# Kernel tuning notes

Measured on AMD Instinct MI355X. Metric: run time of the kernel, lower is better.

## Reference

```python
import jax, jax.numpy as jnp
import numpy as np

N_NODES = 100000
N_EDGES = 1600000
N_FEAT = 512
N_HID = 256
N_CLASS = 40


def setup_inputs() -> dict:
    key = jax.random.key(0)
    ks = jax.random.split(key, 6)
    features = jax.random.normal(ks[0], (N_NODES, N_FEAT), dtype=jnp.float32)
    edge_index = jax.random.randint(ks[1], (2, N_EDGES), 0, N_NODES, dtype=jnp.int32)
    edge_weight = jax.random.uniform(ks[2], (N_EDGES,), dtype=jnp.float32)
    # xavier_uniform with gain=1.414 (as in reset_parameters)
    g = 1.414
    lim1 = g * np.sqrt(6.0 / (N_FEAT + N_HID))
    lim2 = g * np.sqrt(6.0 / (N_HID + N_CLASS))
    W1 = jax.random.uniform(ks[3], (N_FEAT, N_HID), minval=-lim1, maxval=lim1, dtype=jnp.float32)
    W2 = jax.random.uniform(ks[4], (N_HID, N_CLASS), minval=-lim2, maxval=lim2, dtype=jnp.float32)
    b1 = jnp.zeros((N_HID,), dtype=jnp.float32)
    b2 = jnp.zeros((N_CLASS,), dtype=jnp.float32)
    return {"features": features, "edge_index": edge_index, "edge_weight": edge_weight,
            "W1": W1, "b1": b1, "W2": W2, "b2": b2}


def _spmm(edge_index, edge_weight, x, n):
    # out[r] = sum over edges e with row[e]==r of w[e] * x[col[e]]
    row, col = edge_index[0], edge_index[1]
    msgs = edge_weight[:, None] * x[col]  # [E, D]
    return jax.ops.segment_sum(msgs, row, num_segments=n)


def reference(features, edge_index, edge_weight, W1, b1, W2, b2):
    n = features.shape[0]
    # Layer 1: linear -> spmm -> relu (dropout is identity in eval mode)
    h = features @ W1 + b1
    h = jax.nn.relu(_spmm(edge_index, edge_weight, h, n))
    # Layer 2: linear -> spmm -> log_softmax
    h = h @ W2 + b2
    h = _spmm(edge_index, edge_weight, h, n)
    return jax.nn.log_softmax(h, axis=1)
```

## Files before the change

### kernel.cpp

```cpp
#include <hip/hip_runtime.h>
#include <stdint.h>

#define N_NODES 100000
#define N_EDGES 1600000
#define N_FEAT 512
#define N_HID 256
#define N_CLASS 40

typedef float f32x4 __attribute__((ext_vector_type(4)));
typedef __bf16 bf16x8 __attribute__((ext_vector_type(8)));
typedef unsigned short u16x4 __attribute__((ext_vector_type(4)));
typedef unsigned short u16x8 __attribute__((ext_vector_type(8)));

__device__ __forceinline__ unsigned short f2bf(float f) {
  unsigned int u = __float_as_uint(f);
  unsigned int r = (u + 0x7FFFu + ((u >> 16) & 1u)) >> 16;
  return (unsigned short)r;
}
__device__ __forceinline__ float bf2f(unsigned short s) {
  return __uint_as_float(((unsigned int)s) << 16);
}

__global__ void k_w1t(const float* __restrict__ W1, unsigned short* __restrict__ W1t) {
  int gid = blockIdx.x * 256 + threadIdx.x;
  if (gid >= N_HID * N_FEAT) return;
  int n = gid / N_FEAT, k = gid % N_FEAT;
  W1t[gid] = f2bf(W1[(long)k * N_HID + n]);
}

__global__ void k_w2t(const float* __restrict__ W2, unsigned short* __restrict__ W2t) {
  int gid = blockIdx.x * 256 + threadIdx.x;
  if (gid >= 48 * N_HID) return;
  int n = gid / N_HID, k = gid % N_HID;
  W2t[gid] = (n < N_CLASS) ? f2bf(W2[(long)k * N_CLASS + n]) : (unsigned short)0;
}

__global__ void k_hist(const int* __restrict__ ei, int* __restrict__ cnt) {
  int e = blockIdx.x * 256 + threadIdx.x;
  if (e < N_EDGES) atomicAdd(&cnt[ei[e]], 1);
}

__global__ __launch_bounds__(1024) void k_scan_a(const int* __restrict__ cnt,
                                                 int* __restrict__ rp,
                                                 int* __restrict__ bsum) {
  __shared__ int sm[1024];
  const int tid = threadIdx.x;
  const int i = blockIdx.x * 1024 + tid;
  int v = (i < N_NODES) ? cnt[i] : 0;
  sm[tid] = v;
  __syncthreads();
  #pragma unroll
  for (int d = 1; d < 1024; d <<= 1) {
    int t = (tid >= d) ? sm[tid - d] : 0;
    __syncthreads();
    sm[tid] += t;
    __syncthreads();
  }
  if (i < N_NODES) rp[i] = sm[tid] - v;
  if (tid == 1023) bsum[blockIdx.x] = sm[1023];
}

__global__ __launch_bounds__(128) void k_scan_b(const int* __restrict__ bsum,
                                                int* __restrict__ boffs,
                                                int* __restrict__ rp) {
  __shared__ int sm[128];
  const int tid = threadIdx.x;
  const int nb = (N_NODES + 1023) >> 10;
  int v = (tid < nb) ? bsum[tid] : 0;
  sm[tid] = v;
  __syncthreads();
  #pragma unroll
  for (int d = 1; d < 128; d <<= 1) {
    int t = (tid >= d) ? sm[tid - d] : 0;
    __syncthreads();
    sm[tid] += t;
    __syncthreads();
  }
  boffs[tid] = sm[tid] - v;
  if (tid == 127) rp[N_NODES] = sm[127];
}

__global__ void k_scan_c(int* __restrict__ rp, int* __restrict__ cur,
                         const int* __restrict__ boffs) {
  int i = blockIdx.x * 256 + threadIdx.x;
  if (i >= N_NODES) return;
  int v = rp[i] + boffs[i >> 10];
  rp[i] = v;
  cur[i] = v;
}

__global__ void k_scatter(const int* __restrict__ ei, const float* __restrict__ ew,
                          int* __restrict__ cursor, int2* __restrict__ cw) {
  int e = blockIdx.x * 256 + threadIdx.x;
  if (e >= N_EDGES) return;
  int r = ei[e];
  int pos = atomicAdd(&cursor[r], 1);
  cw[pos] = make_int2(ei[N_EDGES + e], __float_as_int(ew[e]));
}

__global__ __launch_bounds__(512) void k_gemm1(const float* __restrict__ X,
                                               const unsigned short* __restrict__ W1t,
                                               const float* __restrict__ b1,
                                               unsigned short* __restrict__ H1) {
  __shared__ unsigned short As[128][32];
  __shared__ unsigned short Bs[256][32];
  const int t = threadIdx.x;
  const int lane = t & 63;
  const int wid = t >> 6;
  const int wm = wid >> 2, wn = wid & 3;
  const long m0 = (long)blockIdx.x * 128;

  f32x4 acc[4][4] = {};
  const int ar = t >> 2;
  const int ak = (t & 3) * 8;
  const long arow = m0 + ar;
  const bool avalid = arow < N_NODES;
  const float* xsrc = X + arow * N_FEAT + ak;
  const unsigned short* bsrc0 = W1t + (long)ar * N_FEAT + ak;
  const unsigned short* bsrc1 = W1t + (long)(ar + 128) * N_FEAT + ak;

  for (int k0 = 0; k0 < N_FEAT; k0 += 32) {
    __syncthreads();
    f32x4 x0 = {}, x1 = {};
    if (avalid) {
      x0 = *(const f32x4*)(xsrc + k0);
      x1 = *(const f32x4*)(xsrc + k0 + 4);
    }
    u16x8 ap;
    ap[0] = f2bf(x0[0]); ap[1] = f2bf(x0[1]); ap[2] = f2bf(x0[2]); ap[3] = f2bf(x0[3]);
    ap[4] = f2bf(x1[0]); ap[5] = f2bf(x1[1]); ap[6] = f2bf(x1[2]); ap[7] = f2bf(x1[3]);
    *(u16x8*)&As[ar][ak] = ap;
    *(u16x8*)&Bs[ar][ak]       = *(const u16x8*)(bsrc0 + k0);
    *(u16x8*)&Bs[ar + 128][ak] = *(const u16x8*)(bsrc1 + k0);
    __syncthreads();

    bf16x8 a[4], b[4];
    #pragma unroll
    for (int mt = 0; mt < 4; ++mt)
      a[mt] = *(const bf16x8*)&As[wm * 64 + mt * 16 + (lane & 15)][(lane >> 4) * 8];
    #pragma unroll
    for (int nt = 0; nt < 4; ++nt)
      b[nt] = *(const bf16x8*)&Bs[wn * 64 + nt * 16 + (lane & 15)][(lane >> 4) * 8];
    #pragma unroll
    for (int mt = 0; mt < 4; ++mt)
      #pragma unroll
      for (int nt = 0; nt < 4; ++nt)
        acc[mt][nt] = __builtin_amdgcn_mfma_f32_16x16x32_bf16(a[mt], b[nt], acc[mt][nt], 0, 0, 0);
  }

  #pragma unroll
  for (int nt = 0; nt < 4; ++nt) {
    int col = wn * 64 + nt * 16 + (lane & 15);
    float bias = b1[col];
    #pragma unroll
    for (int mt = 0; mt < 4; ++mt) {
      #pragma unroll
      for (int i = 0; i < 4; ++i) {
        long row = m0 + wm * 64 + mt * 16 + (lane >> 4) * 4 + i;
        if (row < N_NODES) H1[row * N_HID + col] = f2bf(acc[mt][nt][i] + bias);
      }
    }
  }
}

__global__ __launch_bounds__(256) void k_spmm1(const int* __restrict__ row_ptr,
                                               const int2* __restrict__ cw,
                                               const unsigned short* __restrict__ H1,
                                               unsigned short* __restrict__ H1r) {
  int r = blockIdx.x * 4 + (threadIdx.x >> 6);
  int lane = threadIdx.x & 63;
  if (r >= N_NODES) return;
  int s = row_ptr[r], e = row_ptr[r + 1];
  float a0 = 0.f, a1 = 0.f, a2 = 0.f, a3 = 0.f;
  const unsigned short* Hb = H1 + lane * 4;
  int i = s;
  for (; i + 4 <= e; i += 4) {
    int2 c0 = cw[i + 0];
    int2 c1 = cw[i + 1];
    int2 c2 = cw[i + 2];
    int2 c3 = cw[i + 3];
    u16x4 h0 = *(const u16x4*)(Hb + (long)c0.x * N_HID);
    u16x4 h1 = *(const u16x4*)(Hb + (long)c1.x * N_HID);
    u16x4 h2 = *(const u16x4*)(Hb + (long)c2.x * N_HID);
    u16x4 h3 = *(const u16x4*)(Hb + (long)c3.x * N_HID);
    float w0 = __int_as_float(c0.y);
    float w1 = __int_as_float(c1.y);
    float w2 = __int_as_float(c2.y);
    float w3 = __int_as_float(c3.y);
    a0 += w0 * bf2f(h0[0]); a1 += w0 * bf2f(h0[1]); a2 += w0 * bf2f(h0[2]); a3 += w0 * bf2f(h0[3]);
    a0 += w1 * bf2f(h1[0]); a1 += w1 * bf2f(h1[1]); a2 += w1 * bf2f(h1[2]); a3 += w1 * bf2f(h1[3]);
    a0 += w2 * bf2f(h2[0]); a1 += w2 * bf2f(h2[1]); a2 += w2 * bf2f(h2[2]); a3 += w2 * bf2f(h2[3]);
    a0 += w3 * bf2f(h3[0]); a1 += w3 * bf2f(h3[1]); a2 += w3 * bf2f(h3[2]); a3 += w3 * bf2f(h3[3]);
  }
  for (; i < e; ++i) {
    int2 cwv = cw[i];
    float w = __int_as_float(cwv.y);
    u16x4 hv = *(const u16x4*)(Hb + (long)cwv.x * N_HID);
    a0 += w * bf2f(hv[0]);
    a1 += w * bf2f(hv[1]);
    a2 += w * bf2f(hv[2]);
    a3 += w * bf2f(hv[3]);
  }
  u16x4 o;
  o[0] = f2bf(fmaxf(a0, 0.f));
  o[1] = f2bf(fmaxf(a1, 0.f));
  o[2] = f2bf(fmaxf(a2, 0.f));
  o[3] = f2bf(fmaxf(a3, 0.f));
  *(u16x4*)(H1r + (long)r * N_HID + lane * 4) = o;
}

__global__ __launch_bounds__(256) void k_gemm2(const unsigned short* __restrict__ H1r,
                                               const unsigned short* __restrict__ W2t,
                                               const float* __restrict__ b2,
                                               float* __restrict__ H2) {
  __shared__ unsigned short As[128][32];
  __shared__ unsigned short Bs[48][32];
  const int t = threadIdx.x;
  const int lane = t & 63;
  const int wid = t >> 6;
  const long m0 = (long)blockIdx.x * 128;
  f32x4 acc[2][3] = {};

  for (int k0 = 0; k0 < N_HID; k0 += 32) {
    __syncthreads();
    #pragma unroll
    for (int p = 0; p < 2; ++p) {
      int u = t + p * 256;
      int rr = u >> 2, kk = (u & 3) * 8;
      long gr = m0 + rr;
      u16x8 v = {};
      if (gr < N_NODES) v = *(const u16x8*)(H1r + gr * N_HID + k0 + kk);
      *(u16x8*)&As[rr][kk] = v;
    }
    if (t < 192) {
      int rr = t >> 2, kk = (t & 3) * 8;
      *(u16x8*)&Bs[rr][kk] = *(const u16x8*)(W2t + (long)rr * N_HID + k0 + kk);
    }
    __syncthreads();

    bf16x8 a[2], b[3];
    #pragma unroll
    for (int mt = 0; mt < 2; ++mt)
      a[mt] = *(const bf16x8*)&As[wid * 32 + mt * 16 + (lane & 15)][(lane >> 4) * 8];
    #pragma unroll
    for (int nt = 0; nt < 3; ++nt)
      b[nt] = *(const bf16x8*)&Bs[nt * 16 + (lane & 15)][(lane >> 4) * 8];
    #pragma unroll
    for (int mt = 0; mt < 2; ++mt)
      #pragma unroll
      for (int nt = 0; nt < 3; ++nt)
        acc[mt][nt] = __builtin_amdgcn_mfma_f32_16x16x32_bf16(a[mt], b[nt], acc[mt][nt], 0, 0, 0);
  }

  #pragma unroll
  for (int nt = 0; nt < 3; ++nt) {
    int col = nt * 16 + (lane & 15);
    if (col < N_CLASS) {
      float bias = b2[col];
      #pragma unroll
      for (int mt = 0; mt < 2; ++mt) {
        #pragma unroll
        for (int i = 0; i < 4; ++i) {
          long row = m0 + wid * 32 + mt * 16 + (lane >> 4) * 4 + i;
          if (row < N_NODES) H2[row * N_CLASS + col] = acc[mt][nt][i] + bias;
        }
      }
    }
  }
}

__global__ __launch_bounds__(256) void k_spmm2_lsm(const int* __restrict__ row_ptr,
                                                   const int2* __restrict__ cw,
                                                   const float* __restrict__ H2,
                                                   float* __restrict__ out) {
  int r = blockIdx.x * 4 + (threadIdx.x >> 6);
  int lane = threadIdx.x & 63;
  if (r >= N_NODES) return;
  int s = row_ptr[r], e = row_ptr[r + 1];
  float acc = 0.f;
  const bool act = lane < N_CLASS;
  int i = s;
  for (; i + 4 <= e; i += 4) {
    int2 c0 = cw[i + 0];
    int2 c1 = cw[i + 1];
    int2 c2 = cw[i + 2];
    int2 c3 = cw[i + 3];
    float h0 = 0.f, h1 = 0.f, h2 = 0.f, h3 = 0.f;
    if (act) {
      h0 = H2[(long)c0.x * N_CLASS + lane];
      h1 = H2[(long)c1.x * N_CLASS + lane];
      h2 = H2[(long)c2.x * N_CLASS + lane];
      h3 = H2[(long)c3.x * N_CLASS + lane];
    }
    acc += __int_as_float(c0.y) * h0;
    acc += __int_as_float(c1.y) * h1;
    acc += __int_as_float(c2.y) * h2;
    acc += __int_as_float(c3.y) * h3;
  }
  for (; i < e; ++i) {
    int2 cwv = cw[i];
    if (act) acc += __int_as_float(cwv.y) * H2[(long)cwv.x * N_CLASS + lane];
  }
  float v = act ? acc : -INFINITY;
  float m = v;
  #pragma unroll
  for (int d = 32; d > 0; d >>= 1) m = fmaxf(m, __shfl_xor(m, d));
  float ex = act ? __expf(v - m) : 0.f;
  float ssum = ex;
  #pragma unroll
  for (int d = 32; d > 0; d >>= 1) ssum += __shfl_xor(ssum, d);
  float ls = __logf(ssum);
  if (act) out[(long)r * N_CLASS + lane] = v - m - ls;
}

extern "C" void kernel_launch(void* const* d_in, const int* in_sizes, int n_in,
                              void* d_out, int out_size, void* d_ws, size_t ws_size,
                              hipStream_t stream) {
  (void)in_sizes; (void)n_in; (void)out_size; (void)ws_size;
  const float* X  = (const float*)d_in[0];
  const int*   EI = (const int*)d_in[1];
  const float* EW = (const float*)d_in[2];
  const float* W1 = (const float*)d_in[3];
  const float* b1 = (const float*)d_in[4];
  const float* W2 = (const float*)d_in[5];
  const float* b2 = (const float*)d_in[6];
  float* out = (float*)d_out;

  char* p = (char*)d_ws;
  auto take = [&](size_t bytes) {
    char* r = p;
    p += (bytes + 511) & ~(size_t)511;
    return r;
  };
  unsigned short* W1t   = (unsigned short*)take((size_t)N_HID * N_FEAT * 2);
  unsigned short* W2t   = (unsigned short*)take((size_t)48 * N_HID * 2);
  int*            cnt   = (int*)take((size_t)N_NODES * 4);
  int*            rp    = (int*)take((size_t)(N_NODES + 1) * 4);
  int*            cur   = (int*)take((size_t)(N_NODES + 1) * 4);
  int*            bsum  = (int*)take((size_t)128 * 4);
  int*            boffs = (int*)take((size_t)128 * 4);
  int2*           cw    = (int2*)take((size_t)N_EDGES * 8);
  unsigned short* H1    = (unsigned short*)take((size_t)N_NODES * N_HID * 2);
  unsigned short* H1r   = (unsigned short*)take((size_t)N_NODES * N_HID * 2);
  float*          H2    = (float*)take((size_t)N_NODES * N_CLASS * 4);

  const int NB_SCAN = (N_NODES + 1023) / 1024;

  hipMemsetAsync(cnt, 0, (size_t)N_NODES * 4, stream);
  k_w1t<<<(N_HID * N_FEAT + 255) / 256, 256, 0, stream>>>(W1, W1t);
  k_w2t<<<(48 * N_HID + 255) / 256, 256, 0, stream>>>(W2, W2t);
  k_hist<<<(N_EDGES + 255) / 256, 256, 0, stream>>>(EI, cnt);
  k_scan_a<<<NB_SCAN, 1024, 0, stream>>>(cnt, rp, bsum);
  k_scan_b<<<1, 128, 0, stream>>>(bsum, boffs, rp);
  k_scan_c<<<(N_NODES + 255) / 256, 256, 0, stream>>>(rp, cur, boffs);
  k_scatter<<<(N_EDGES + 255) / 256, 256, 0, stream>>>(EI, EW, cur, cw);
  k_gemm1<<<(N_NODES + 127) / 128, 512, 0, stream>>>(X, W1t, b1, H1);
  k_spmm1<<<(N_NODES + 3) / 4, 256, 0, stream>>>(rp, cw, H1, H1r);
  k_gemm2<<<(N_NODES + 127) / 128, 256, 0, stream>>>(H1r, W2t, b2, H2);
  k_spmm2_lsm<<<(N_NODES + 3) / 4, 256, 0, stream>>>(rp, cw, H2, out);
}
```

Baseline: 471.9 us.

## Fuse preprocessing kernels, record atomic ranks, overlap edge scatter with GEMM1

Merges the weight transposes and the histogram into one launch, and the histogram now records each edge's atomic rank. The scatter then needs no second atomic pass and runs as odd blocks interleaved with the GEMM1 blocks in one fused kernel. GEMM1 gains register prefetch of the next K slice and padded LDS rows to reduce bank conflicts, and spmm1 unrolls to 8 edges. H2 is padded to a 48-float stride. In exchange, a rank array is added and the fused kernel has divergent block roles sharing one resource footprint.

Result: faster. 437.8 us (-7.2%).

```diff
diff --git a/kernel.cpp b/kernel.cpp
--- a/kernel.cpp
+++ b/kernel.cpp
@@ -6,6 +6,7 @@
 #define N_FEAT 512
 #define N_HID 256
 #define N_CLASS 40
+#define H2S 48
 
 typedef float f32x4 __attribute__((ext_vector_type(4)));
 typedef __bf16 bf16x8 __attribute__((ext_vector_type(8)));
@@ -21,23 +22,32 @@
   return __uint_as_float(((unsigned int)s) << 16);
 }
 
-__global__ void k_w1t(const float* __restrict__ W1, unsigned short* __restrict__ W1t) {
-  int gid = blockIdx.x * 256 + threadIdx.x;
-  if (gid >= N_HID * N_FEAT) return;
-  int n = gid / N_FEAT, k = gid % N_FEAT;
-  W1t[gid] = f2bf(W1[(long)k * N_HID + n]);
-}
-
-__global__ void k_w2t(const float* __restrict__ W2, unsigned short* __restrict__ W2t) {
-  int gid = blockIdx.x * 256 + threadIdx.x;
-  if (gid >= 48 * N_HID) return;
-  int n = gid / N_HID, k = gid % N_HID;
-  W2t[gid] = (n < N_CLASS) ? f2bf(W2[(long)k * N_CLASS + n]) : (unsigned short)0;
-}
-
-__global__ void k_hist(const int* __restrict__ ei, int* __restrict__ cnt) {
-  int e = blockIdx.x * 256 + threadIdx.x;
-  if (e < N_EDGES) atomicAdd(&cnt[ei[e]], 1);
+#define HIST_BLOCKS 1563
+#define W1T_BLOCKS  512
+#define W2T_BLOCKS  48
+__global__ __launch_bounds__(256) void k_pre(const float* __restrict__ W1,
+                                             const float* __restrict__ W2,
+                                             const int* __restrict__ ei,
+                                             unsigned short* __restrict__ W1t,
+                                             unsigned short* __restrict__ W2t,
+                                             int* __restrict__ cnt,
+                                             int* __restrict__ rank) {
+  const int bid = blockIdx.x, tid = threadIdx.x;
+  if (bid < HIST_BLOCKS) {
+    #pragma unroll
+    for (int k = 0; k < 4; ++k) {
+      int e = bid * 1024 + k * 256 + tid;
+      if (e < N_EDGES) rank[e] = atomicAdd(&cnt[ei[e]], 1);
+    }
+  } else if (bid < HIST_BLOCKS + W1T_BLOCKS) {
+    int gid = (bid - HIST_BLOCKS) * 256 + tid;
+    int n = gid >> 9, k = gid & 511;
+    W1t[gid] = f2bf(W1[(long)k * N_HID + n]);
+  } else {
+    int gid = (bid - HIST_BLOCKS - W1T_BLOCKS) * 256 + tid;
+    int n = gid >> 8, k = gid & 255;
+    W2t[gid] = (n < N_CLASS) ? f2bf(W2[(long)k * N_CLASS + n]) : (unsigned short)0;
+  }
 }
 
 __global__ __launch_bounds__(1024) void k_scan_a(const int* __restrict__ cnt,
@@ -80,59 +90,76 @@
   if (tid == 127) rp[N_NODES] = sm[127];
 }
 
-__global__ void k_scan_c(int* __restrict__ rp, int* __restrict__ cur,
-                         const int* __restrict__ boffs) {
+__global__ void k_scan_c(int* __restrict__ rp, const int* __restrict__ boffs) {
   int i = blockIdx.x * 256 + threadIdx.x;
   if (i >= N_NODES) return;
-  int v = rp[i] + boffs[i >> 10];
-  rp[i] = v;
-  cur[i] = v;
-}
-
-__global__ void k_scatter(const int* __restrict__ ei, const float* __restrict__ ew,
-                          int* __restrict__ cursor, int2* __restrict__ cw) {
-  int e = blockIdx.x * 256 + threadIdx.x;
-  if (e >= N_EDGES) return;
-  int r = ei[e];
-  int pos = atomicAdd(&cursor[r], 1);
-  cw[pos] = make_int2(ei[N_EDGES + e], __float_as_int(ew[e]));
-}
-
-__global__ __launch_bounds__(512) void k_gemm1(const float* __restrict__ X,
-                                               const unsigned short* __restrict__ W1t,
-                                               const float* __restrict__ b1,
-                                               unsigned short* __restrict__ H1) {
-  __shared__ unsigned short As[128][32];
-  __shared__ unsigned short Bs[256][32];
+  rp[i] += boffs[i >> 10];
+}
+
+#define NG1 782
+__global__ __launch_bounds__(512) void k_fused1(const float* __restrict__ X,
+                                                const unsigned short* __restrict__ W1t,
+                                                const float* __restrict__ b1,
+                                                unsigned short* __restrict__ H1,
+                                                const int* __restrict__ ei,
+                                                const float* __restrict__ ew,
+                                                const int* __restrict__ rank,
+                                                const int* __restrict__ rp,
+                                                int2* __restrict__ cw) {
+  __shared__ unsigned short As[128][40];
+  __shared__ unsigned short Bs[256][40];
   const int t = threadIdx.x;
+
+  if (blockIdx.x & 1) {
+    int sb = blockIdx.x >> 1;
+    #pragma unroll
+    for (int k = 0; k < 4; ++k) {
+      int e = sb * 2048 + k * 512 + t;
+      if (e < N_EDGES) {
+        int r = ei[e];
+        int pos = rp[r] + rank[e];
+        cw[pos] = make_int2(ei[N_EDGES + e], __float_as_int(ew[e]));
+      }
+    }
+    return;
+  }
+
+  const int gb = blockIdx.x >> 1;
   const int lane = t & 63;
   const int wid = t >> 6;
   const int wm = wid >> 2, wn = wid & 3;
-  const long m0 = (long)blockIdx.x * 128;
+  const long m0 = (long)gb * 128;
 
   f32x4 acc[4][4] = {};
   const int ar = t >> 2;
   const int ak = (t & 3) * 8;
   const long arow = m0 + ar;
   const bool avalid = arow < N_NODES;
-  const float* xsrc = X + arow * N_FEAT + ak;
-  const unsigned short* bsrc0 = W1t + (long)ar * N_FEAT + ak;
-  const unsigned short* bsrc1 = W1t + (long)(ar + 128) * N_FEAT + ak;
+  const float* xs = X + arow * N_FEAT;
+  const unsigned short* ws0 = W1t + (long)ar * N_FEAT;
+  const unsigned short* ws1 = W1t + (long)(ar + 128) * N_FEAT;
+
+  f32x4 xa = {}, xb = {};
+  if (avalid) { xa = *(const f32x4*)(xs + ak); xb = *(const f32x4*)(xs + ak + 4); }
+  u16x8 wa = *(const u16x8*)(ws0 + ak);
+  u16x8 wb = *(const u16x8*)(ws1 + ak);
 
   for (int k0 = 0; k0 < N_FEAT; k0 += 32) {
     __syncthreads();
-    f32x4 x0 = {}, x1 = {};
-    if (avalid) {
-      x0 = *(const f32x4*)(xsrc + k0);
-      x1 = *(const f32x4*)(xsrc + k0 + 4);
-    }
     u16x8 ap;
-    ap[0] = f2bf(x0[0]); ap[1] = f2bf(x0[1]); ap[2] = f2bf(x0[2]); ap[3] = f2bf(x0[3]);
-    ap[4] = f2bf(x1[0]); ap[5] = f2bf(x1[1]); ap[6] = f2bf(x1[2]); ap[7] = f2bf(x1[3]);
+    ap[0] = f2bf(xa[0]); ap[1] = f2bf(xa[1]); ap[2] = f2bf(xa[2]); ap[3] = f2bf(xa[3]);
+    ap[4] = f2bf(xb[0]); ap[5] = f2bf(xb[1]); ap[6] = f2bf(xb[2]); ap[7] = f2bf(xb[3]);
     *(u16x8*)&As[ar][ak] = ap;
-    *(u16x8*)&Bs[ar][ak]       = *(const u16x8*)(bsrc0 + k0);
-    *(u16x8*)&Bs[ar + 128][ak] = *(const u16x8*)(bsrc1 + k0);
-    __syncthreads();
+    *(u16x8*)&Bs[ar][ak] = wa;
+    *(u16x8*)&Bs[ar + 128][ak] = wb;
+    __syncthreads();
+
+    if (k0 + 32 < N_FEAT) {
+      int ko = k0 + 32 + ak;
+      if (avalid) { xa = *(const f32x4*)(xs + ko); xb = *(const f32x4*)(xs + ko + 4); }
+      wa = *(const u16x8*)(ws0 + ko);
+      wb = *(const u16x8*)(ws1 + ko);
+    }
 
     bf16x8 a[4], b[4];
     #pragma unroll
@@ -174,23 +201,29 @@
   float a0 = 0.f, a1 = 0.f, a2 = 0.f, a3 = 0.f;
   const unsigned short* Hb = H1 + lane * 4;
   int i = s;
-  for (; i + 4 <= e; i += 4) {
-    int2 c0 = cw[i + 0];
-    int2 c1 = cw[i + 1];
-    int2 c2 = cw[i + 2];
-    int2 c3 = cw[i + 3];
+  for (; i + 8 <= e; i += 8) {
+    int2 c0 = cw[i + 0]; int2 c1 = cw[i + 1]; int2 c2 = cw[i + 2]; int2 c3 = cw[i + 3];
+    int2 c4 = cw[i + 4]; int2 c5 = cw[i + 5]; int2 c6 = cw[i + 6]; int2 c7 = cw[i + 7];
     u16x4 h0 = *(const u16x4*)(Hb + (long)c0.x * N_HID);
     u16x4 h1 = *(const u16x4*)(Hb + (long)c1.x * N_HID);
     u16x4 h2 = *(const u16x4*)(Hb + (long)c2.x * N_HID);
     u16x4 h3 = *(const u16x4*)(Hb + (long)c3.x * N_HID);
-    float w0 = __int_as_float(c0.y);
-    float w1 = __int_as_float(c1.y);
-    float w2 = __int_as_float(c2.y);
-    float w3 = __int_as_float(c3.y);
+    u16x4 h4 = *(const u16x4*)(Hb + (long)c4.x * N_HID);
+    u16x4 h5 = *(const u16x4*)(Hb + (long)c5.x * N_HID);
+    u16x4 h6 = *(const u16x4*)(Hb + (long)c6.x * N_HID);
+    u16x4 h7 = *(const u16x4*)(Hb + (long)c7.x * N_HID);
+    float w0 = __int_as_float(c0.y), w1 = __int_as_float(c1.y);
+    float w2 = __int_as_float(c2.y), w3 = __int_as_float(c3.y);
+    float w4 = __int_as_float(c4.y), w5 = __int_as_float(c5.y);
+    float w6 = __int_as_float(c6.y), w7 = __int_as_float(c7.y);
     a0 += w0 * bf2f(h0[0]); a1 += w0 * bf2f(h0[1]); a2 += w0 * bf2f(h0[2]); a3 += w0 * bf2f(h0[3]);
     a0 += w1 * bf2f(h1[0]); a1 += w1 * bf2f(h1[1]); a2 += w1 * bf2f(h1[2]); a3 += w1 * bf2f(h1[3]);
     a0 += w2 * bf2f(h2[0]); a1 += w2 * bf2f(h2[1]); a2 += w2 * bf2f(h2[2]); a3 += w2 * bf2f(h2[3]);
     a0 += w3 * bf2f(h3[0]); a1 += w3 * bf2f(h3[1]); a2 += w3 * bf2f(h3[2]); a3 += w3 * bf2f(h3[3]);
+    a0 += w4 * bf2f(h4[0]); a1 += w4 * bf2f(h4[1]); a2 += w4 * bf2f(h4[2]); a3 += w4 * bf2f(h4[3]);
+    a0 += w5 * bf2f(h5[0]); a1 += w5 * bf2f(h5[1]); a2 += w5 * bf2f(h5[2]); a3 += w5 * bf2f(h5[3]);
+    a0 += w6 * bf2f(h6[0]); a1 += w6 * bf2f(h6[1]); a2 += w6 * bf2f(h6[2]); a3 += w6 * bf2f(h6[3]);
+    a0 += w7 * bf2f(h7[0]); a1 += w7 * bf2f(h7[1]); a2 += w7 * bf2f(h7[2]); a3 += w7 * bf2f(h7[3]);
   }
   for (; i < e; ++i) {
     int2 cwv = cw[i];
@@ -213,8 +246,8 @@
                                                const unsigned short* __restrict__ W2t,
                                                const float* __restrict__ b2,
                                                float* __restrict__ H2) {
-  __shared__ unsigned short As[128][32];
-  __shared__ unsigned short Bs[48][32];
+  __shared__ unsigned short As[128][40];
+  __shared__ unsigned short Bs[48][40];
   const int t = threadIdx.x;
   const int lane = t & 63;
   const int wid = t >> 6;
@@ -262,7 +295,7 @@
         #pragma unroll
         for (int i = 0; i < 4; ++i) {
           long row = m0 + wid * 32 + mt * 16 + (lane >> 4) * 4 + i;
-          if (row < N_NODES) H2[row * N_CLASS + col] = acc[mt][nt][i] + bias;
+          if (row < N_NODES) H2[row * H2S + col] = acc[mt][nt][i] + bias;
         }
       }
     }
@@ -287,10 +320,10 @@
     int2 c3 = cw[i + 3];
     float h0 = 0.f, h1 = 0.f, h2 = 0.f, h3 = 0.f;
     if (act) {
-      h0 = H2[(long)c0.x * N_CLASS + lane];
-      h1 = H2[(long)c1.x * N_CLASS + lane];
-      h2 = H2[(long)c2.x * N_CLASS + lane];
-      h3 = H2[(long)c3.x * N_CLASS + lane];
+      h0 = H2[(long)c0.x * H2S + lane];
+      h1 = H2[(long)c1.x * H2S + lane];
+      h2 = H2[(long)c2.x * H2S + lane];
+      h3 = H2[(long)c3.x * H2S + lane];
     }
     acc += __int_as_float(c0.y) * h0;
     acc += __int_as_float(c1.y) * h1;
@@ -299,7 +332,7 @@
   }
   for (; i < e; ++i) {
     int2 cwv = cw[i];
-    if (act) acc += __int_as_float(cwv.y) * H2[(long)cwv.x * N_CLASS + lane];
+    if (act) acc += __int_as_float(cwv.y) * H2[(long)cwv.x * H2S + lane];
   }
   float v = act ? acc : -INFINITY;
   float m = v;
@@ -336,25 +369,22 @@
   unsigned short* W2t   = (unsigned short*)take((size_t)48 * N_HID * 2);
   int*            cnt   = (int*)take((size_t)N_NODES * 4);
   int*            rp    = (int*)take((size_t)(N_NODES + 1) * 4);
-  int*            cur   = (int*)take((size_t)(N_NODES + 1) * 4);
   int*            bsum  = (int*)take((size_t)128 * 4);
   int*            boffs = (int*)take((size_t)128 * 4);
+  int*            rank  = (int*)take((size_t)N_EDGES * 4);
   int2*           cw    = (int2*)take((size_t)N_EDGES * 8);
   unsigned short* H1    = (unsigned short*)take((size_t)N_NODES * N_HID * 2);
   unsigned short* H1r   = (unsigned short*)take((size_t)N_NODES * N_HID * 2);
-  float*          H2    = (float*)take((size_t)N_NODES * N_CLASS * 4);
+  float*          H2    = (float*)take((size_t)N_NODES * H2S * 4);
 
   const int NB_SCAN = (N_NODES + 1023) / 1024;
 
   hipMemsetAsync(cnt, 0, (size_t)N_NODES * 4, stream);
-  k_w1t<<<(N_HID * N_FEAT + 255) / 256, 256, 0, stream>>>(W1, W1t);
-  k_w2t<<<(48 * N_HID + 255) / 256, 256, 0, stream>>>(W2, W2t);
-  k_hist<<<(N_EDGES + 255) / 256, 256, 0, stream>>>(EI, cnt);
+  k_pre<<<HIST_BLOCKS + W1T_BLOCKS + W2T_BLOCKS, 256, 0, stream>>>(W1, W2, EI, W1t, W2t, cnt, rank);
   k_scan_a<<<NB_SCAN, 1024, 0, stream>>>(cnt, rp, bsum);
   k_scan_b<<<1, 128, 0, stream>>>(bsum, boffs, rp);
-  k_scan_c<<<(N_NODES + 255) / 256, 256, 0, stream>>>(rp, cur, boffs);
-  k_scatter<<<(N_EDGES + 255) / 256, 256, 0, stream>>>(EI, EW, cur, cw);
-  k_gemm1<<<(N_NODES + 127) / 128, 512, 0, stream>>>(X, W1t, b1, H1);
+  k_scan_c<<<(N_NODES + 255) / 256, 256, 0, stream>>>(rp, boffs);
+  k_fused1<<<2 * NG1, 512, 0, stream>>>(X, W1t, b1, H1, EI, EW, rank, rp, cw);
   k_spmm1<<<(N_NODES + 3) / 4, 256, 0, stream>>>(rp, cw, H1, H1r);
   k_gemm2<<<(N_NODES + 127) / 128, 256, 0, stream>>>(H1r, W2t, b2, H2);
   k_spmm2_lsm<<<(N_NODES + 3) / 4, 256, 0, stream>>>(rp, cw, H2, out);
```
